# Kernel tuning notes

Measured on AMD Instinct MI355X. Metric: run time of the kernel, lower is better.

## Reference

```python
import jax, jax.numpy as jnp
import numpy as np

B, C, T, H, W = 32, 384, 16, 14, 14
K, NUM_SAMPLES, SIGMA = 8, 1000, 0.05
C2 = 2 * C  # ScoreNet doubles embed_dim internally


def setup_inputs() -> dict:
    key = jax.random.key(0)
    ks = jax.random.split(key, 12)
    def rn(k, shape, s=0.02):
        return jax.random.normal(k, shape, dtype=jnp.float32) * s
    return {
        "frames": jax.random.normal(ks[0], (B, C, T, H, W), dtype=jnp.float32),
        "noise": jax.random.normal(ks[1], (B, NUM_SAMPLES, T), dtype=jnp.float32),
        "conv_w": rn(ks[2], (C, C, 1, 3, 3)),
        "conv_b": jnp.zeros((C,), jnp.float32),
        "bn_g": jnp.ones((C,), jnp.float32),
        "bn_b": jnp.zeros((C,), jnp.float32),
        "ln_g": jnp.ones((C2,), jnp.float32),
        "ln_b": jnp.zeros((C2,), jnp.float32),
        "lin_w": rn(ks[3], (C2, C2)),
        "lin_b": jnp.zeros((C2,), jnp.float32),
        "w1": rn(ks[4], (C2, C)), "b1": jnp.zeros((C,), jnp.float32),
        "w2": rn(ks[5], (C, C // 2)), "b2": jnp.zeros((C // 2,), jnp.float32),
        "w3": rn(ks[6], (C // 2, 1)), "b3": jnp.zeros((1,), jnp.float32),
    }


def score_net(frames, conv_w, conv_b, bn_g, bn_b, ln_g, ln_b, lin_w, lin_b,
              w1, b1, w2, b2, w3, b3):
    x = jax.lax.stop_gradient(frames)  # ScoreNet detaches its input
    x = jax.lax.conv_general_dilated(
        x, conv_w, window_strides=(1, 2, 2), padding='VALID',
        dimension_numbers=('NCDHW', 'OIDHW', 'NCDHW'))
    x = x + conv_b[None, :, None, None, None]
    # BatchNorm3d in training mode: biased batch stats over (N,T,H,W)
    m = x.mean(axis=(0, 2, 3, 4))
    v = x.var(axis=(0, 2, 3, 4))
    x = (x - m[None, :, None, None, None]) / jnp.sqrt(v + 1e-5)[None, :, None, None, None]
    x = x * bn_g[None, :, None, None, None] + bn_b[None, :, None, None, None]
    # b c t h w -> b t (h w) c
    b, c, t, h, w = x.shape
    x = jnp.transpose(x, (0, 2, 3, 4, 1)).reshape(b, t, h * w, c)
    x = jnp.concatenate([x.mean(axis=2), x.max(axis=2)], axis=-1)  # [B,T,2C]
    # LayerNorm(2C)
    mu = x.mean(-1, keepdims=True)
    var = x.var(-1, keepdims=True)
    x = (x - mu) / jnp.sqrt(var + 1e-5) * ln_g + ln_b
    x = jax.nn.gelu(x @ lin_w + lin_b, approximate=False)
    local_x = x[..., :C2 // 2]
    global_x = jnp.broadcast_to(x[..., C2 // 2:].mean(axis=1, keepdims=True), (b, t, C2 // 2))
    x = jnp.concatenate([local_x, global_x], axis=-1)
    x = jax.nn.gelu(x @ w1 + b1, approximate=False)
    x = jax.nn.gelu(x @ w2 + b2, approximate=False)
    score = (x @ w3 + b3)[..., 0]  # [B,T]
    smin = score.min(axis=-1, keepdims=True)
    smax = score.max(axis=-1, keepdims=True)
    return (score - smin) / (smax - smin + 1e-5)


def perturbed_indicators(score, noise):
    d = score.shape[-1]
    pert = score[:, None, :] + noise * SIGMA  # [B,N,T]
    idx_top = jnp.sort(jax.lax.top_k(pert, K)[1], axis=-1)        # [B,N,K]
    idx_back = jnp.sort(jax.lax.top_k(-pert, d - K)[1], axis=-1)  # [B,N,T-K]
    ind_top = jax.nn.one_hot(idx_top, d, dtype=jnp.float32).mean(axis=1)   # [B,K,T]
    ind_back = jax.nn.one_hot(idx_back, d, dtype=jnp.float32).mean(axis=1)  # [B,T-K,T]
    return ind_top, ind_back


def reference(frames, noise, conv_w, conv_b, bn_g, bn_b, ln_g, ln_b, lin_w, lin_b,
              w1, b1, w2, b2, w3, b3):
    score = score_net(frames, conv_w, conv_b, bn_g, bn_b, ln_g, ln_b, lin_w, lin_b,
                      w1, b1, w2, b2, w3, b3)  # [B,T]
    ind_top, ind_back = perturbed_indicators(score, noise)
    # b c t h w -> b t (h w c)
    flat = jnp.transpose(frames, (0, 2, 3, 4, 1)).reshape(B, T, H * W * C)
    p_top = jnp.einsum('bkd,bdc->bkc', ind_top, flat)
    p_back = jnp.einsum('bkd,bdc->bkc', ind_back, flat)
    frames_topk = jnp.transpose(p_top.reshape(B, K, H, W, C), (0, 4, 1, 2, 3))
    frames_back = jnp.transpose(p_back.reshape(B, T - K, H, W, C), (0, 4, 1, 2, 3))
    sorted_inds = jnp.argsort(score, axis=1)
    return frames_topk, frames_back, sorted_inds
```

## Files before the change

kernel.cpp:

```cpp
#include <hip/hip_runtime.h>
#include <hip/hip_bf16.h>
#include <cstdint>

#define NB 32
#define NC 384
#define NT 16
#define NH 14
#define NW 14
#define HWI 196
#define HOW 6
#define HWO 36
#define C2 768
#define MCONV (NB*NT*HWO)
#define KCONV 3456
#define TOPK 8
#define NSAMP 1000
#define OUT_TOPK_ELEMS (NB*NC*TOPK*HWI)
#define OUT_INDS_OFF   (2*OUT_TOPK_ELEMS)
#define PELEMS (MCONV*NC)

#define OFF_FHI  0ull
#define OFF_FLO  77070336ull
#define OFF_WHI  154140672ull
#define OFF_WLO  156794880ull
#define OFF_CONV 159449088ull
#define OFF_PART 0ull
#define OFF_BNSC 442368ull
#define OFF_BNSH 443904ull
#define OFF_Y    445440ull
#define OFF_X1   2018304ull
#define OFF_GM   3591168ull
#define OFF_H1   3640320ull
#define OFF_H2   4426752ull
#define OFF_IND  4819968ull

typedef __attribute__((ext_vector_type(4))) float f32x4;
typedef __attribute__((ext_vector_type(8))) short bf16x8;

__device__ __forceinline__ unsigned short f2bf(float f) {
  unsigned u = __float_as_uint(f);
  unsigned r = (u + 0x7FFFu + ((u >> 16) & 1u)) >> 16;
  return (unsigned short)r;
}
__device__ __forceinline__ float bf2f(unsigned short u) {
  return __uint_as_float(((unsigned)u) << 16);
}

__device__ __forceinline__ void gload_lds16(const void* gptr, void* lptr) {
  __builtin_amdgcn_global_load_lds(
      (const __attribute__((address_space(1))) unsigned int*)gptr,
      (__attribute__((address_space(3))) unsigned int*)lptr, 16, 0, 0);
}

__global__ __launch_bounds__(256)
void split_frames(const float* __restrict__ fr,
                  unsigned short* __restrict__ fhi,
                  unsigned short* __restrict__ flo) {
  __shared__ unsigned int tile[64][197];
  int bid = blockIdx.x;
  int cb = bid % 6, bt = bid / 6;
  int b = bt >> 4, t = bt & 15;
  const float* src = fr + (((size_t)b * NC + cb * 64) * NT + t) * HWI;
  for (int i = threadIdx.x; i < 64 * 49; i += 256) {
    int c = i / 49, q = i - c * 49;
    float4 v = *(const float4*)(src + (size_t)c * (NT * HWI) + q * 4);
    float vv[4] = {v.x, v.y, v.z, v.w};
#pragma unroll
    for (int u = 0; u < 4; ++u) {
      unsigned short h = f2bf(vv[u]);
      unsigned short l = f2bf(vv[u] - bf2f(h));
      tile[c][q * 4 + u] = ((unsigned)h << 16) | (unsigned)l;
    }
  }
  __syncthreads();
  size_t obase = ((size_t)bt * HWI) * NC + cb * 64;
  for (int i = threadIdx.x; i < 196 * 8; i += 256) {
    int hw = i >> 3, c8 = i & 7;
    bf16x8 vh, vl;
#pragma unroll
    for (int u = 0; u < 8; ++u) {
      unsigned p = tile[c8 * 8 + u][hw];
      vh[u] = (short)(p >> 16);
      vl[u] = (short)(p & 0xffff);
    }
    size_t o = obase + (size_t)hw * NC + c8 * 8;
    *(bf16x8*)(fhi + o) = vh;
    *(bf16x8*)(flo + o) = vl;
  }
}

__global__ __launch_bounds__(256)
void split_w(const float* __restrict__ cw,
             unsigned short* __restrict__ whi,
             unsigned short* __restrict__ wlo) {
  __shared__ float t[KCONV];
  int co = blockIdx.x;
  const float* src = cw + (size_t)co * KCONV;
  for (int i = threadIdx.x; i < KCONV / 4; i += 256)
    *(float4*)&t[i * 4] = *(const float4*)&src[i * 4];
  __syncthreads();
  unsigned short* oh = whi + (size_t)co * KCONV;
  unsigned short* ol = wlo + (size_t)co * KCONV;
  for (int i = threadIdx.x; i < KCONV; i += 256) {
    int c9 = i / NC, ci = i - c9 * NC;
    float v = t[ci * 9 + c9];
    unsigned short h = f2bf(v);
    oh[i] = h; ol[i] = f2bf(v - bf2f(h));
  }
}

__global__ __launch_bounds__(256, 4)
void conv_gemm(const unsigned short* __restrict__ fhi,
               const unsigned short* __restrict__ flo,
               const unsigned short* __restrict__ whi,
               const unsigned short* __restrict__ wlo,
               const float* __restrict__ conv_b,
               float* __restrict__ p0, float* __restrict__ p1,
               float* __restrict__ p2, float* __restrict__ p3) {
  __shared__ unsigned short sAhi[128 * 32], sAlo[128 * 32];
  __shared__ unsigned short sBhi[128 * 32], sBlo[128 * 32];
  const int tid = threadIdx.x;
  const int lane = tid & 63;
  const int wv = tid >> 6;
  const int bid = blockIdx.x;
  const int bm = bid % 144;
  const int r  = bid / 144;
  const int bn = r % 3;
  const int kz = r / 3;

  int aoff[2], boff[2];
#pragma unroll
  for (int j = 0; j < 2; ++j) {
    int l = (wv * 2 + j) * 64 + lane;
    int row = l >> 2;
    int chunk = (l & 3) ^ ((l >> 3) & 3);
    int m = bm * 128 + row;
    int wo = m % 6; int tmp = m / 6;
    int ho = tmp % 6; tmp /= 6;
    aoff[j] = ((tmp * HWI) + (2 * ho) * NW + 2 * wo) * NC + chunk * 8;
    int co = bn * 128 + row;
    boff[j] = co * KCONV + chunk * 8;
  }

  f32x4 acc[4][4];
#pragma unroll
  for (int i = 0; i < 4; ++i)
#pragma unroll
    for (int j = 0; j < 4; ++j) acc[i][j] = (f32x4){0.f, 0.f, 0.f, 0.f};

  const int wrow = (wv >> 1) * 64;
  const int wcol = (wv & 1) * 64;
  const int fr_row = lane & 15;
  const int slot8 = (((lane >> 4) ^ ((fr_row >> 1) & 3))) * 8;

  int c9  = (kz * 27) / 12;
  int rem = (kz * 27) % 12;
  for (int s = 0; s < 27; ++s) {
    int kh = c9 / 3, kw = c9 - kh * 3;
    int soffA = (kh * NW + kw) * NC + rem * 32;
    int soffB = c9 * NC + rem * 32;
#pragma unroll
    for (int j = 0; j < 2; ++j) {
      char* ldsA  = (char*)sAhi + (wv * 2 + j) * 1024;
      char* ldsAl = (char*)sAlo + (wv * 2 + j) * 1024;
      char* ldsB  = (char*)sBhi + (wv * 2 + j) * 1024;
      char* ldsBl = (char*)sBlo + (wv * 2 + j) * 1024;
      gload_lds16(fhi + aoff[j] + soffA, ldsA);
      gload_lds16(flo + aoff[j] + soffA, ldsAl);
      gload_lds16(whi + boff[j] + soffB, ldsB);
      gload_lds16(wlo + boff[j] + soffB, ldsBl);
    }
    __syncthreads();
    bf16x8 ah[4], al[4], bh[4], bl[4];
#pragma unroll
    for (int m = 0; m < 4; ++m) {
      int rr = wrow + m * 16 + fr_row;
      ah[m] = *(const bf16x8*)&sAhi[rr * 32 + slot8];
      al[m] = *(const bf16x8*)&sAlo[rr * 32 + slot8];
    }
#pragma unroll
    for (int n = 0; n < 4; ++n) {
      int rr = wcol + n * 16 + fr_row;
      bh[n] = *(const bf16x8*)&sBhi[rr * 32 + slot8];
      bl[n] = *(const bf16x8*)&sBlo[rr * 32 + slot8];
    }
#pragma unroll
    for (int m = 0; m < 4; ++m)
#pragma unroll
      for (int n = 0; n < 4; ++n) {
        acc[m][n] = __builtin_amdgcn_mfma_f32_16x16x32_bf16(ah[m], bh[n], acc[m][n], 0, 0, 0);
        acc[m][n] = __builtin_amdgcn_mfma_f32_16x16x32_bf16(ah[m], bl[n], acc[m][n], 0, 0, 0);
        acc[m][n] = __builtin_amdgcn_mfma_f32_16x16x32_bf16(al[m], bh[n], acc[m][n], 0, 0, 0);
      }
    __syncthreads();
    if (++rem == 12) { rem = 0; ++c9; }
  }

  float* dst = (kz == 0) ? p0 : (kz == 1) ? p1 : (kz == 2) ? p2 : p3;
#pragma unroll
  for (int m = 0; m < 4; ++m)
#pragma unroll
    for (int n = 0; n < 4; ++n) {
      int col = bn * 128 + wcol + n * 16 + (lane & 15);
      float cb = (kz == 0) ? conv_b[col] : 0.f;
#pragma unroll
      for (int j = 0; j < 4; ++j) {
        int row = bm * 128 + wrow + m * 16 + (lane >> 4) * 4 + j;
        dst[(size_t)row * NC + col] = acc[m][n][j] + cb;
      }
    }
}

__global__ __launch_bounds__(384)
void bn_part(float* __restrict__ p0, const float* __restrict__ p1,
             const float* __restrict__ p2, const float* __restrict__ p3,
             float* __restrict__ part) {
  int c = threadIdx.x;
  int r0 = blockIdx.x * 128;
  float s = 0.f, sq = 0.f;
  for (int r = 0; r < 128; ++r) {
    size_t off = (size_t)(r0 + r) * NC + c;
    float v = p0[off] + p1[off] + p2[off] + p3[off];
    p0[off] = v;
    s += v; sq += v * v;
  }
  part[blockIdx.x * 768 + c] = s;
  part[blockIdx.x * 768 + 384 + c] = sq;
}

__global__ __launch_bounds__(384)
void bn_fin(const float* __restrict__ part, const float* __restrict__ bn_g,
            const float* __restrict__ bn_b, float* __restrict__ bnsc,
            float* __restrict__ bnsh) {
  int c = threadIdx.x;
  float s = 0.f, sq = 0.f;
  for (int i = 0; i < 144; ++i) {
    s += part[i * 768 + c];
    sq += part[i * 768 + 384 + c];
  }
  float mean = s / (float)MCONV;
  float var = sq / (float)MCONV - mean * mean;
  float sc = bn_g[c] / sqrtf(var + 1e-5f);
  bnsc[c] = sc;
  bnsh[c] = bn_b[c] - mean * sc;
}

__global__ __launch_bounds__(384)
void pool_ln(const float* __restrict__ csum,
             const float* __restrict__ bnsc,
             const float* __restrict__ bnsh, const float* __restrict__ ln_g,
             const float* __restrict__ ln_b, float* __restrict__ y) {
  __shared__ float r1[384], r2[384], stats[2];
  int bt = blockIdx.x, c = threadIdx.x;
  float sc = bnsc[c], sh = bnsh[c];
  size_t base = (size_t)bt * HWO * NC + c;
  float sum = 0.f, mx = -1e30f;
  for (int hw = 0; hw < HWO; ++hw) {
    float v = csum[base + (size_t)hw * NC] * sc + sh;
    sum += v;
    mx = fmaxf(mx, v);
  }
  float meanv = sum * (1.f / 36.f);
  r1[c] = meanv + mx;
  r2[c] = meanv * meanv + mx * mx;
  __syncthreads();
  for (int s = 192; s >= 6; s >>= 1) {
    if (c < s) { r1[c] += r1[c + s]; r2[c] += r2[c + s]; }
    __syncthreads();
  }
  if (c == 0) {
    float S1 = 0.f, S2 = 0.f;
    for (int i = 0; i < 6; ++i) { S1 += r1[i]; S2 += r2[i]; }
    float mu = S1 / (float)C2;
    float var = S2 / (float)C2 - mu * mu;
    stats[0] = mu;
    stats[1] = 1.0f / sqrtf(var + 1e-5f);
  }
  __syncthreads();
  float mu = stats[0], rstd = stats[1];
  y[(size_t)bt * C2 + c] = (meanv - mu) * rstd * ln_g[c] + ln_b[c];
  y[(size_t)bt * C2 + 384 + c] = (mx - mu) * rstd * ln_g[384 + c] + ln_b[384 + c];
}

template <int GELU, int X2>
__global__ __launch_bounds__(256)
void gemm64(const float* __restrict__ A, const float* __restrict__ gmv,
            const float* __restrict__ Wm,
            const float* __restrict__ bias, float* __restrict__ Cm,
            int K, int N) {
  __shared__ float As[64][17];
  __shared__ float Bs[16][68];
  int tid = threadIdx.x;
  int tx = tid & 15, ty = tid >> 4;
  int m0 = blockIdx.y * 64, n0 = blockIdx.x * 64;
  int ar = tid >> 2, ak = (tid & 3) * 4;
  int br = tid >> 4, bc = (tid & 15) * 4;
  float acc[4][4] = {};
  for (int kt = 0; kt < K; kt += 16) {
    int kcol = kt + ak;
    float4 av;
    if (X2 && kcol >= 384)
      av = *(const float4*)(gmv + ((m0 + ar) >> 4) * 384 + (kcol - 384));
    else
      av = *(const float4*)(A + (size_t)(m0 + ar) * K + kcol);
    float4 bv = *(const float4*)(Wm + (size_t)(kt + br) * N + n0 + bc);
    As[ar][ak + 0] = av.x; As[ar][ak + 1] = av.y;
    As[ar][ak + 2] = av.z; As[ar][ak + 3] = av.w;
    Bs[br][bc + 0] = bv.x; Bs[br][bc + 1] = bv.y;
    Bs[br][bc + 2] = bv.z; Bs[br][bc + 3] = bv.w;
    __syncthreads();
#pragma unroll
    for (int kk = 0; kk < 16; ++kk) {
      float a0 = As[ty * 4 + 0][kk], a1 = As[ty * 4 + 1][kk];
      float a2 = As[ty * 4 + 2][kk], a3 = As[ty * 4 + 3][kk];
      float b0 = Bs[kk][tx * 4 + 0], b1 = Bs[kk][tx * 4 + 1];
      float b2 = Bs[kk][tx * 4 + 2], b3 = Bs[kk][tx * 4 + 3];
      acc[0][0] += a0 * b0; acc[0][1] += a0 * b1; acc[0][2] += a0 * b2; acc[0][3] += a0 * b3;
      acc[1][0] += a1 * b0; acc[1][1] += a1 * b1; acc[1][2] += a1 * b2; acc[1][3] += a1 * b3;
      acc[2][0] += a2 * b0; acc[2][1] += a2 * b1; acc[2][2] += a2 * b2; acc[2][3] += a2 * b3;
      acc[3][0] += a3 * b0; acc[3][1] += a3 * b1; acc[3][2] += a3 * b2; acc[3][3] += a3 * b3;
    }
    __syncthreads();
  }
#pragma unroll
  for (int i = 0; i < 4; ++i) {
    int row = m0 + ty * 4 + i;
#pragma unroll
    for (int j = 0; j < 4; ++j) {
      int col = n0 + tx * 4 + j;
      float v = acc[i][j] + bias[col];
      if (GELU) v = 0.5f * v * (1.0f + erff(v * 0.70710678118654752f));
      Cm[(size_t)row * N + col] = v;
    }
  }
}

__global__ __launch_bounds__(384)
void gmean_k(const float* __restrict__ x1, float* __restrict__ gm) {
  int b = blockIdx.x, c = threadIdx.x;
  float s = 0.f;
  for (int t = 0; t < NT; ++t) s += x1[((size_t)b * NT + t) * C2 + 384 + c];
  gm[b * 384 + c] = s * (1.f / 16.f);
}

__global__ __launch_bounds__(256)
void score_head(const float* __restrict__ h2, const float* __restrict__ w3,
                const float* __restrict__ b3, const float* __restrict__ noise,
                unsigned* __restrict__ pcnt, float* __restrict__ out_inds) {
  int b = blockIdx.x >> 3, chunk = blockIdx.x & 7;
  int tid = threadIdx.x;
  int lane = tid & 63, wv = tid >> 6;
  __shared__ float sv[16], sn[16];
  __shared__ unsigned cnt[256];
  for (int t = wv; t < 16; t += 4) {
    const float* hr = h2 + ((size_t)b * 16 + t) * 192;
    float p = 0.f;
    for (int i = lane; i < 192; i += 64) p += hr[i] * w3[i];
#pragma unroll
    for (int off = 32; off; off >>= 1) p += __shfl_down(p, off, 64);
    if (lane == 0) sv[t] = p + b3[0];
  }
  cnt[tid] = 0;
  __syncthreads();
  if (tid == 0) {
    float mn = sv[0], mx = sv[0];
    for (int t = 1; t < 16; ++t) { mn = fminf(mn, sv[t]); mx = fmaxf(mx, sv[t]); }
    float inv = 1.0f / (mx - mn + 1e-5f);
    for (int t = 0; t < 16; ++t) sn[t] = (sv[t] - mn) * inv;
  }
  __syncthreads();
  if (chunk == 0 && tid < 16) {
    int t = tid, r = 0;
    for (int u = 0; u < 16; ++u)
      r += (sv[u] < sv[t]) || (sv[u] == sv[t] && u < t);
    out_inds[b * 16 + r] = (float)t;
  }
  if (tid < 125) {
    int s = chunk * 125 + tid;
    const float* nz = noise + ((size_t)b * NSAMP + s) * 16;
    float pert[16];
#pragma unroll
    for (int t = 0; t < 16; ++t) pert[t] = sn[t] + 0.05f * nz[t];
    unsigned tm = 0, bm2 = 0;
#pragma unroll
    for (int t = 0; t < 16; ++t) {
      int ct = 0, cb = 0;
#pragma unroll
      for (int u = 0; u < 16; ++u) {
        ct += (pert[u] > pert[t]) || (pert[u] == pert[t] && u < t);
        cb += (pert[u] < pert[t]) || (pert[u] == pert[t] && u < t);
      }
      if (ct < 8) tm |= 1u << t;
      if (cb < 8) bm2 |= 1u << t;
    }
    int j = 0, jb = 0;
#pragma unroll
    for (int t = 0; t < 16; ++t) {
      if (tm & (1u << t)) { if (j < 8) atomicAdd(&cnt[j * 16 + t], 1u); ++j; }
      if (bm2 & (1u << t)) { if (jb < 8) atomicAdd(&cnt[128 + jb * 16 + t], 1u); ++jb; }
    }
  }
  __syncthreads();
  pcnt[(size_t)(b * 8 + chunk) * 256 + tid] = cnt[tid];
}

__global__ __launch_bounds__(256)
void gather_k(const float* __restrict__ frames, const unsigned* __restrict__ pcnt,
              float* __restrict__ out) {
  int bid = blockIdx.x;
  int tid = threadIdx.x;
  int b = (bid * 4) / NC;
  __shared__ float wt[256];
  {
    unsigned s = 0;
    const unsigned* pc = pcnt + (size_t)b * 8 * 256 + tid;
#pragma unroll
    for (int ch = 0; ch < 8; ++ch) s += pc[ch * 256];
    wt[tid] = (float)s / 1000.0f;
  }
  __syncthreads();
  if (tid >= 196) return;
  int cc = tid / 49, q = tid - cc * 49;
  int bc = bid * 4 + cc;
  const float4* src = (const float4*)(frames + (size_t)bc * NT * HWI) + q;
  float4 v[16];
#pragma unroll
  for (int t = 0; t < 16; ++t) v[t] = src[t * 49];
  float4* o1 = (float4*)(out + (size_t)bc * TOPK * HWI) + q;
  float4* o2 = (float4*)(out + OUT_TOPK_ELEMS + (size_t)bc * TOPK * HWI) + q;
#pragma unroll
  for (int k = 0; k < TOPK; ++k) {
    float4 st = {0.f, 0.f, 0.f, 0.f}, sb = {0.f, 0.f, 0.f, 0.f};
#pragma unroll
    for (int t = 0; t < 16; ++t) {
      float a = wt[k * 16 + t], bw = wt[128 + k * 16 + t];
      st.x += a * v[t].x; st.y += a * v[t].y; st.z += a * v[t].z; st.w += a * v[t].w;
      sb.x += bw * v[t].x; sb.y += bw * v[t].y; sb.z += bw * v[t].z; sb.w += bw * v[t].w;
    }
    o1[k * 49] = st;
    o2[k * 49] = sb;
  }
}

extern "C" void kernel_launch(void* const* d_in, const int* in_sizes, int n_in,
                              void* d_out, int out_size, void* d_ws, size_t ws_size,
                              hipStream_t stream) {
  const float* frames = (const float*)d_in[0];
  const float* noise  = (const float*)d_in[1];
  const float* conv_w = (const float*)d_in[2];
  const float* conv_b = (const float*)d_in[3];
  const float* bn_g   = (const float*)d_in[4];
  const float* bn_b   = (const float*)d_in[5];
  const float* ln_g   = (const float*)d_in[6];
  const float* ln_b   = (const float*)d_in[7];
  const float* lin_w  = (const float*)d_in[8];
  const float* lin_b  = (const float*)d_in[9];
  const float* w1     = (const float*)d_in[10];
  const float* b1     = (const float*)d_in[11];
  const float* w2     = (const float*)d_in[12];
  const float* b2     = (const float*)d_in[13];
  const float* w3     = (const float*)d_in[14];
  const float* b3     = (const float*)d_in[15];

  char* ws = (char*)d_ws;
  unsigned short* fhi = (unsigned short*)(ws + OFF_FHI);
  unsigned short* flo = (unsigned short*)(ws + OFF_FLO);
  unsigned short* whi = (unsigned short*)(ws + OFF_WHI);
  unsigned short* wlo = (unsigned short*)(ws + OFF_WLO);
  float* p0    = (float*)(ws + OFF_CONV);
  float* part  = (float*)(ws + OFF_PART);
  float* bnsc  = (float*)(ws + OFF_BNSC);
  float* bnsh  = (float*)(ws + OFF_BNSH);
  float* y     = (float*)(ws + OFF_Y);
  float* x1    = (float*)(ws + OFF_X1);
  float* gm    = (float*)(ws + OFF_GM);
  float* h1    = (float*)(ws + OFF_H1);
  float* h2    = (float*)(ws + OFF_H2);
  unsigned* pcnt = (unsigned*)(ws + OFF_IND);
  float* out   = (float*)d_out;
  float* p1    = out;
  float* p2    = out + PELEMS;
  float* p3    = out + 2 * (size_t)PELEMS;

  split_frames<<<3072, 256, 0, stream>>>(frames, fhi, flo);
  split_w<<<384, 256, 0, stream>>>(conv_w, whi, wlo);
  conv_gemm<<<1728, 256, 0, stream>>>(fhi, flo, whi, wlo, conv_b, p0, p1, p2, p3);
  bn_part<<<144, 384, 0, stream>>>(p0, p1, p2, p3, part);
  bn_fin<<<1, 384, 0, stream>>>(part, bn_g, bn_b, bnsc, bnsh);
  pool_ln<<<512, 384, 0, stream>>>(p0, bnsc, bnsh, ln_g, ln_b, y);
  gemm64<1, 0><<<dim3(12, 8), 256, 0, stream>>>(y, nullptr, lin_w, lin_b, x1, 768, 768);
  gmean_k<<<32, 384, 0, stream>>>(x1, gm);
  gemm64<1, 1><<<dim3(6, 8), 256, 0, stream>>>(x1, gm, w1, b1, h1, 768, 384);
  gemm64<1, 0><<<dim3(3, 8), 256, 0, stream>>>(h1, nullptr, w2, b2, h2, 384, 192);
  score_head<<<256, 256, 0, stream>>>(h2, w3, b3, noise, pcnt, out + OUT_INDS_OFF);
  gather_k<<<3072, 256, 0, stream>>>(frames, pcnt, out);
}
```

Before: 502.1 us.

## Merge split kernels, fold global mean into GEMM epilogue, simplify score_head

Merges the frame and weight bf16 split kernels into one launch, and folds the per-batch global mean into the epilogue of the first GEMM so the separate gmean kernel is gone. pool_ln now reduces with wavefront shuffles instead of a shared-memory tree. score_head runs one block per batch that loops over all samples and writes normalized indicator weights directly, so gather_k no longer sums partial counts. The aim is fewer launches and less small-kernel overhead, but score_head now uses only 32 blocks, which cuts its parallelism.

```diff
diff --git a/kernel.cpp b/kernel.cpp
--- a/kernel.cpp
+++ b/kernel.cpp
@@ -53,59 +53,57 @@
 }
 
 __global__ __launch_bounds__(256)
-void split_frames(const float* __restrict__ fr,
-                  unsigned short* __restrict__ fhi,
-                  unsigned short* __restrict__ flo) {
-  __shared__ unsigned int tile[64][197];
+void split_all(const float* __restrict__ fr, const float* __restrict__ cw,
+               unsigned short* __restrict__ fhi, unsigned short* __restrict__ flo,
+               unsigned short* __restrict__ whi, unsigned short* __restrict__ wlo) {
+  __shared__ char smem[64 * 197 * 4];
   int bid = blockIdx.x;
-  int cb = bid % 6, bt = bid / 6;
-  int b = bt >> 4, t = bt & 15;
-  const float* src = fr + (((size_t)b * NC + cb * 64) * NT + t) * HWI;
-  for (int i = threadIdx.x; i < 64 * 49; i += 256) {
-    int c = i / 49, q = i - c * 49;
-    float4 v = *(const float4*)(src + (size_t)c * (NT * HWI) + q * 4);
-    float vv[4] = {v.x, v.y, v.z, v.w};
-#pragma unroll
-    for (int u = 0; u < 4; ++u) {
-      unsigned short h = f2bf(vv[u]);
-      unsigned short l = f2bf(vv[u] - bf2f(h));
-      tile[c][q * 4 + u] = ((unsigned)h << 16) | (unsigned)l;
-    }
-  }
-  __syncthreads();
-  size_t obase = ((size_t)bt * HWI) * NC + cb * 64;
-  for (int i = threadIdx.x; i < 196 * 8; i += 256) {
-    int hw = i >> 3, c8 = i & 7;
-    bf16x8 vh, vl;
-#pragma unroll
-    for (int u = 0; u < 8; ++u) {
-      unsigned p = tile[c8 * 8 + u][hw];
-      vh[u] = (short)(p >> 16);
-      vl[u] = (short)(p & 0xffff);
-    }
-    size_t o = obase + (size_t)hw * NC + c8 * 8;
-    *(bf16x8*)(fhi + o) = vh;
-    *(bf16x8*)(flo + o) = vl;
-  }
-}
-
-__global__ __launch_bounds__(256)
-void split_w(const float* __restrict__ cw,
-             unsigned short* __restrict__ whi,
-             unsigned short* __restrict__ wlo) {
-  __shared__ float t[KCONV];
-  int co = blockIdx.x;
-  const float* src = cw + (size_t)co * KCONV;
-  for (int i = threadIdx.x; i < KCONV / 4; i += 256)
-    *(float4*)&t[i * 4] = *(const float4*)&src[i * 4];
-  __syncthreads();
-  unsigned short* oh = whi + (size_t)co * KCONV;
-  unsigned short* ol = wlo + (size_t)co * KCONV;
-  for (int i = threadIdx.x; i < KCONV; i += 256) {
-    int c9 = i / NC, ci = i - c9 * NC;
-    float v = t[ci * 9 + c9];
-    unsigned short h = f2bf(v);
-    oh[i] = h; ol[i] = f2bf(v - bf2f(h));
+  if (bid < 3072) {
+    unsigned int (*tile)[197] = (unsigned int (*)[197])smem;
+    int cb = bid % 6, bt = bid / 6;
+    int b = bt >> 4, t = bt & 15;
+    const float* src = fr + (((size_t)b * NC + cb * 64) * NT + t) * HWI;
+    for (int i = threadIdx.x; i < 64 * 49; i += 256) {
+      int c = i / 49, q = i - c * 49;
+      float4 v = *(const float4*)(src + (size_t)c * (NT * HWI) + q * 4);
+      float vv[4] = {v.x, v.y, v.z, v.w};
+#pragma unroll
+      for (int u = 0; u < 4; ++u) {
+        unsigned short h = f2bf(vv[u]);
+        unsigned short l = f2bf(vv[u] - bf2f(h));
+        tile[c][q * 4 + u] = ((unsigned)h << 16) | (unsigned)l;
+      }
+    }
+    __syncthreads();
+    size_t obase = ((size_t)bt * HWI) * NC + cb * 64;
+    for (int i = threadIdx.x; i < 196 * 8; i += 256) {
+      int hw = i >> 3, c8 = i & 7;
+      bf16x8 vh, vl;
+#pragma unroll
+      for (int u = 0; u < 8; ++u) {
+        unsigned p = tile[c8 * 8 + u][hw];
+        vh[u] = (short)(p >> 16);
+        vl[u] = (short)(p & 0xffff);
+      }
+      size_t o = obase + (size_t)hw * NC + c8 * 8;
+      *(bf16x8*)(fhi + o) = vh;
+      *(bf16x8*)(flo + o) = vl;
+    }
+  } else {
+    float* t = (float*)smem;
+    int co = bid - 3072;
+    const float* src = cw + (size_t)co * KCONV;
+    for (int i = threadIdx.x; i < KCONV / 4; i += 256)
+      *(float4*)&t[i * 4] = *(const float4*)&src[i * 4];
+    __syncthreads();
+    unsigned short* oh = whi + (size_t)co * KCONV;
+    unsigned short* ol = wlo + (size_t)co * KCONV;
+    for (int i = threadIdx.x; i < KCONV; i += 256) {
+      int c9 = i / NC, ci = i - c9 * NC;
+      float v = t[ci * 9 + c9];
+      unsigned short h = f2bf(v);
+      oh[i] = h; ol[i] = f2bf(v - bf2f(h));
+    }
   }
 }
 
@@ -250,26 +248,30 @@
              const float* __restrict__ bnsc,
              const float* __restrict__ bnsh, const float* __restrict__ ln_g,
              const float* __restrict__ ln_b, float* __restrict__ y) {
-  __shared__ float r1[384], r2[384], stats[2];
+  __shared__ float r1[6], r2[6], stats[2];
   int bt = blockIdx.x, c = threadIdx.x;
   float sc = bnsc[c], sh = bnsh[c];
   size_t base = (size_t)bt * HWO * NC + c;
   float sum = 0.f, mx = -1e30f;
+#pragma unroll
   for (int hw = 0; hw < HWO; ++hw) {
     float v = csum[base + (size_t)hw * NC] * sc + sh;
     sum += v;
     mx = fmaxf(mx, v);
   }
   float meanv = sum * (1.f / 36.f);
-  r1[c] = meanv + mx;
-  r2[c] = meanv * meanv + mx * mx;
-  __syncthreads();
-  for (int s = 192; s >= 6; s >>= 1) {
-    if (c < s) { r1[c] += r1[c + s]; r2[c] += r2[c + s]; }
-    __syncthreads();
-  }
+  float v1 = meanv + mx;
+  float v2 = meanv * meanv + mx * mx;
+#pragma unroll
+  for (int off = 32; off; off >>= 1) {
+    v1 += __shfl_down(v1, off, 64);
+    v2 += __shfl_down(v2, off, 64);
+  }
+  if ((c & 63) == 0) { r1[c >> 6] = v1; r2[c >> 6] = v2; }
+  __syncthreads();
   if (c == 0) {
     float S1 = 0.f, S2 = 0.f;
+#pragma unroll
     for (int i = 0; i < 6; ++i) { S1 += r1[i]; S2 += r2[i]; }
     float mu = S1 / (float)C2;
     float var = S2 / (float)C2 - mu * mu;
@@ -282,14 +284,15 @@
   y[(size_t)bt * C2 + 384 + c] = (mx - mu) * rstd * ln_g[384 + c] + ln_b[384 + c];
 }
 
-template <int GELU, int X2>
+template <int GELU, int X2, int GM>
 __global__ __launch_bounds__(256)
 void gemm64(const float* __restrict__ A, const float* __restrict__ gmv,
             const float* __restrict__ Wm,
             const float* __restrict__ bias, float* __restrict__ Cm,
-            int K, int N) {
+            int K, int N, float* __restrict__ gmout) {
   __shared__ float As[64][17];
   __shared__ float Bs[16][68];
+  __shared__ float gmred[16][64];
   int tid = threadIdx.x;
   int tx = tid & 15, ty = tid >> 4;
   int m0 = blockIdx.y * 64, n0 = blockIdx.x * 64;
@@ -322,6 +325,7 @@
     }
     __syncthreads();
   }
+  float vout[4][4];
 #pragma unroll
   for (int i = 0; i < 4; ++i) {
     int row = m0 + ty * 4 + i;
@@ -330,24 +334,27 @@
       int col = n0 + tx * 4 + j;
       float v = acc[i][j] + bias[col];
       if (GELU) v = 0.5f * v * (1.0f + erff(v * 0.70710678118654752f));
+      vout[i][j] = v;
       Cm[(size_t)row * N + col] = v;
     }
   }
-}
-
-__global__ __launch_bounds__(384)
-void gmean_k(const float* __restrict__ x1, float* __restrict__ gm) {
-  int b = blockIdx.x, c = threadIdx.x;
-  float s = 0.f;
-  for (int t = 0; t < NT; ++t) s += x1[((size_t)b * NT + t) * C2 + 384 + c];
-  gm[b * 384 + c] = s * (1.f / 16.f);
+  if (GM && n0 >= 384) {
+#pragma unroll
+    for (int j = 0; j < 4; ++j)
+      gmred[ty][tx * 4 + j] = vout[0][j] + vout[1][j] + vout[2][j] + vout[3][j];
+    __syncthreads();
+    int b_l = tid >> 6, col = tid & 63;
+    float g = (gmred[b_l * 4 + 0][col] + gmred[b_l * 4 + 1][col] +
+               gmred[b_l * 4 + 2][col] + gmred[b_l * 4 + 3][col]) * (1.f / 16.f);
+    gmout[(blockIdx.y * 4 + b_l) * 384 + (n0 - 384) + col] = g;
+  }
 }
 
 __global__ __launch_bounds__(256)
 void score_head(const float* __restrict__ h2, const float* __restrict__ w3,
                 const float* __restrict__ b3, const float* __restrict__ noise,
-                unsigned* __restrict__ pcnt, float* __restrict__ out_inds) {
-  int b = blockIdx.x >> 3, chunk = blockIdx.x & 7;
+                float* __restrict__ ind, float* __restrict__ out_inds) {
+  int b = blockIdx.x;
   int tid = threadIdx.x;
   int lane = tid & 63, wv = tid >> 6;
   __shared__ float sv[16], sn[16];
@@ -369,14 +376,13 @@
     for (int t = 0; t < 16; ++t) sn[t] = (sv[t] - mn) * inv;
   }
   __syncthreads();
-  if (chunk == 0 && tid < 16) {
+  if (tid < 16) {
     int t = tid, r = 0;
     for (int u = 0; u < 16; ++u)
       r += (sv[u] < sv[t]) || (sv[u] == sv[t] && u < t);
     out_inds[b * 16 + r] = (float)t;
   }
-  if (tid < 125) {
-    int s = chunk * 125 + tid;
+  for (int s = tid; s < NSAMP; s += 256) {
     const float* nz = noise + ((size_t)b * NSAMP + s) * 16;
     float pert[16];
 #pragma unroll
@@ -401,23 +407,17 @@
     }
   }
   __syncthreads();
-  pcnt[(size_t)(b * 8 + chunk) * 256 + tid] = cnt[tid];
+  ind[b * 256 + tid] = (float)cnt[tid] / 1000.0f;
 }
 
 __global__ __launch_bounds__(256)
-void gather_k(const float* __restrict__ frames, const unsigned* __restrict__ pcnt,
+void gather_k(const float* __restrict__ frames, const float* __restrict__ ind,
               float* __restrict__ out) {
   int bid = blockIdx.x;
   int tid = threadIdx.x;
   int b = (bid * 4) / NC;
   __shared__ float wt[256];
-  {
-    unsigned s = 0;
-    const unsigned* pc = pcnt + (size_t)b * 8 * 256 + tid;
-#pragma unroll
-    for (int ch = 0; ch < 8; ++ch) s += pc[ch * 256];
-    wt[tid] = (float)s / 1000.0f;
-  }
+  wt[tid] = ind[b * 256 + tid];
   __syncthreads();
   if (tid >= 196) return;
   int cc = tid / 49, q = tid - cc * 49;
@@ -476,22 +476,20 @@
   float* gm    = (float*)(ws + OFF_GM);
   float* h1    = (float*)(ws + OFF_H1);
   float* h2    = (float*)(ws + OFF_H2);
-  unsigned* pcnt = (unsigned*)(ws + OFF_IND);
+  float* ind   = (float*)(ws + OFF_IND);
   float* out   = (float*)d_out;
   float* p1    = out;
   float* p2    = out + PELEMS;
   float* p3    = out + 2 * (size_t)PELEMS;
 
-  split_frames<<<3072, 256, 0, stream>>>(frames, fhi, flo);
-  split_w<<<384, 256, 0, stream>>>(conv_w, whi, wlo);
+  split_all<<<3456, 256, 0, stream>>>(frames, conv_w, fhi, flo, whi, wlo);
   conv_gemm<<<1728, 256, 0, stream>>>(fhi, flo, whi, wlo, conv_b, p0, p1, p2, p3);
   bn_part<<<144, 384, 0, stream>>>(p0, p1, p2, p3, part);
   bn_fin<<<1, 384, 0, stream>>>(part, bn_g, bn_b, bnsc, bnsh);
   pool_ln<<<512, 384, 0, stream>>>(p0, bnsc, bnsh, ln_g, ln_b, y);
-  gemm64<1, 0><<<dim3(12, 8), 256, 0, stream>>>(y, nullptr, lin_w, lin_b, x1, 768, 768);
-  gmean_k<<<32, 384, 0, stream>>>(x1, gm);
-  gemm64<1, 1><<<dim3(6, 8), 256, 0, stream>>>(x1, gm, w1, b1, h1, 768, 384);
-  gemm64<1, 0><<<dim3(3, 8), 256, 0, stream>>>(h1, nullptr, w2, b2, h2, 384, 192);
-  score_head<<<256, 256, 0, stream>>>(h2, w3, b3, noise, pcnt, out + OUT_INDS_OFF);
-  gather_k<<<3072, 256, 0, stream>>>(frames, pcnt, out);
-}
+  gemm64<1, 0, 1><<<dim3(12, 8), 256, 0, stream>>>(y, nullptr, lin_w, lin_b, x1, 768, 768, gm);
+  gemm64<1, 1, 0><<<dim3(6, 8), 256, 0, stream>>>(x1, gm, w1, b1, h1, 768, 384, nullptr);
+  gemm64<1, 0, 0><<<dim3(3, 8), 256, 0, stream>>>(h1, nullptr, w2, b2, h2, 384, 192, nullptr);
+  score_head<<<32, 256, 0, stream>>>(h2, w3, b3, noise, ind, out + OUT_INDS_OFF);
+  gather_k<<<3072, 256, 0, stream>>>(frames, ind, out);
+}
```

Result: no change. 508.8 us (+1.3%).
